# Optimization experiments

Hardware: AMD Instinct MI355X
Metric: run time of the kernel (lower is better)

Reference implementation:

```python
import jax, jax.numpy as jnp
import numpy as np

# Model dims: n_layers, window, n_head, d_head, d_model, d_ff, num_cls, mel_channels, T
L_, W_, H_, DH_ = 8, 32, 8, 64
D_ = H_ * DH_
DFF_, C_, M_, T_ = 2048, 256, 80, 512


def _ln(x, w, b, eps=1e-5):
    mu = x.mean()
    var = ((x - mu) ** 2).mean()
    return (x - mu) * jax.lax.rsqrt(var + eps) * w + b


def setup_inputs() -> dict:
    key = jax.random.key(0)
    ks = jax.random.split(key, 12)
    s = 0.02
    def w(k, shape):
        return jax.random.normal(k, shape, dtype=jnp.float32) * s
    return {
        "y": jax.random.normal(ks[0], (M_, T_), dtype=jnp.float32),
        "samples": jax.random.uniform(ks[1], (T_,), dtype=jnp.float32),
        "emb": jax.random.normal(ks[2], (C_, D_), dtype=jnp.float32),
        "cond_W": w(ks[3], (D_, M_)),
        "ln_w": jnp.ones((L_, D_), jnp.float32),
        "ln_b": jnp.zeros((L_, D_), jnp.float32),
        "kv_w": w(ks[4], (L_, 2 * D_, D_)),
        "kv_b": jnp.zeros((L_, 2 * D_), jnp.float32),
        "q_w": w(ks[5], (L_, D_, D_)),
        "q_b": jnp.zeros((L_, D_), jnp.float32),
        "o_w": w(ks[6], (L_, D_, D_)),
        "o_b": jnp.zeros((L_, D_), jnp.float32),
        "fln_w": jnp.ones((L_, D_), jnp.float32),
        "fln_b": jnp.zeros((L_, D_), jnp.float32),
        "ff_w1": w(ks[7], (L_, DFF_, D_)),
        "ff_b1": jnp.zeros((L_, DFF_), jnp.float32),
        "ff_w2": w(ks[8], (L_, D_, DFF_)),
        "ff_b2": jnp.zeros((L_, D_), jnp.float32),
        "head_r": w(ks[9], (L_, W_, H_, DH_)),
        "last_w": w(ks[10], (C_, D_)),
        "last_b": jnp.zeros((C_,), jnp.float32),
    }


def _decode(y, samples, emb, cond_W, ln_w, ln_b, kv_w, kv_b, q_w, q_b, o_w, o_b,
            fln_w, fln_b, ff_w1, ff_b1, ff_w2, ff_b2, head_r, last_w, last_b):
    L, W, H, Dh = head_r.shape
    D = H * Dh
    C = last_w.shape[0]
    scale = 1.0 / float(np.sqrt(Dh))
    emb_t = jnp.tanh(emb)                 # buffer 'emb' is emb.tanh()
    ycond = (cond_W @ y).T                # [T, D]
    T = ycond.shape[0]
    x0 = emb_t[C // 2 - 1]
    buf0 = jnp.zeros((L, W, 2 * D), ycond.dtype)  # fixed-size rolling KV cache, newest at the end
    layer_params = (ln_w, ln_b, kv_w, kv_b, q_w, q_b, o_w, o_b,
                    fln_w, fln_b, ff_w1, ff_b1, ff_w2, ff_b2, head_r)

    def time_step(carry, ts):
        x, bufs = carry
        cond, sample, t = ts
        # slot w is valid iff it holds a real token: right-aligned, min(t+1, W) valid
        valid = jnp.arange(W) >= (W - 1 - t)

        def layer_step(xc, lp):
            (lw, lb, kw, kb, qw, qb, ow, ob, fw, fb, w1, b1, w2, b2, r, buf) = lp
            xc = cond + xc
            tmp = _ln(xc, lw, lb)
            hkv = kw @ tmp + kb                               # [2D]
            hq = (qw @ tmp + qb).reshape(H, Dh)               # [H, Dh]
            buf = jnp.concatenate([buf[1:], hkv[None]], 0)    # roll cache, [W, 2D]
            k, v = jnp.split(buf, 2, axis=1)
            k = k.reshape(W, H, Dh) + r                       # head_r right-aligned with cache
            v = v.reshape(W, H, Dh)
            scores = jnp.einsum('whd,hd->hw', k, hq) * scale
            scores = jnp.where(valid[None, :], scores, -jnp.inf)
            attn = jax.nn.softmax(scores, axis=1)
            out = jnp.einsum('hw,whd->hd', attn, v).reshape(D)
            xc = ow @ out + ob + xc
            h = jax.nn.gelu(w1 @ _ln(xc, fw, fb) + b1)
            xc = xc + w2 @ h + b2
            return xc, buf

        x, newbufs = jax.lax.scan(layer_step, x, layer_params + (bufs,))
        logits = last_w @ x + last_b                          # c = 1.0
        cum = jnp.cumsum(jax.nn.softmax(logits), axis=0)
        idx = jnp.argmax(cum > sample)                        # first index where cum > u
        return (emb_t[idx], newbufs), (idx, logits)

    (_, _), (outputs, logits) = jax.lax.scan(
        time_step, (x0, buf0), (ycond, samples, jnp.arange(T)))
    return outputs, logits


def reference(y, samples, emb, cond_W, ln_w, ln_b, kv_w, kv_b, q_w, q_b, o_w, o_b,
              fln_w, fln_b, ff_w1, ff_b1, ff_w2, ff_b2, head_r, last_w, last_b):
    outputs, _ = _decode(y, samples, emb, cond_W, ln_w, ln_b, kv_w, kv_b, q_w, q_b,
                         o_w, o_b, fln_w, fln_b, ff_w1, ff_b1, ff_w2, ff_b2,
                         head_r, last_w, last_b)
    return outputs
```

## Files before the change

### kernel.cpp

```cpp
#include <hip/hip_runtime.h>
#include <math.h>

#define LAYERS 8
#define WIN    32
#define NH     8
#define DHD    64
#define DM     512
#define DFF    2048
#define NCLS   256
#define MEL    80
#define TT     512

#define GRID   256
#define BLK    256

#define KVROW  1056

typedef unsigned int  u32;
typedef unsigned long long u64;

__device__ inline float wredsum(float v){
#pragma unroll
  for (int m = 32; m >= 1; m >>= 1) v += __shfl_xor(v, m, 64);
  return v;
}
__device__ inline float wredmax(float v){
#pragma unroll
  for (int m = 32; m >= 1; m >>= 1) v = fmaxf(v, __shfl_xor(v, m, 64));
  return v;
}

__device__ inline float ld_sc(float* p){
  return __hip_atomic_load(p, __ATOMIC_RELAXED, __HIP_MEMORY_SCOPE_AGENT);
}
__device__ inline void st_sc(float* p, float v){
  __hip_atomic_store(p, v, __ATOMIC_RELAXED, __HIP_MEMORY_SCOPE_AGENT);
}
__device__ inline float2 ld_sc2(float* p){
  u64 u = __hip_atomic_load((u64*)p, __ATOMIC_RELAXED, __HIP_MEMORY_SCOPE_AGENT);
  union { u64 u; float2 f; } cv; cv.u = u; return cv.f;
}

__device__ inline float dot512(const float* w, const float* vec, int lane){
  float4 a0 = *(const float4*)(w + 4*lane);
  float4 a1 = *(const float4*)(w + 256 + 4*lane);
  float4 b0 = *(const float4*)(vec + 4*lane);
  float4 b1 = *(const float4*)(vec + 256 + 4*lane);
  float p = a0.x*b0.x + a0.y*b0.y + a0.z*b0.z + a0.w*b0.w
          + a1.x*b1.x + a1.y*b1.y + a1.z*b1.z + a1.w*b1.w;
  return wredsum(p);
}

__device__ inline float gelu_tanh(float x){
  float x3 = x*x*x;
  return 0.5f*x*(1.0f + tanhf(0.7978845608028654f*(x + 0.044715f*x3)));
}

__device__ inline void bar_arrive(u32* flags, int b, int ph){
  __syncthreads();
  if (threadIdx.x == 0)
    __hip_atomic_store(flags + b, (u32)ph, __ATOMIC_RELAXED, __HIP_MEMORY_SCOPE_AGENT);
}
__device__ inline void bar_wait(u32* flags, int ph){
  int tid = threadIdx.x;
  if (tid < 64){
    u64* fp = (u64*)flags + 2*tid;
    for (;;){
      u64 v0 = __hip_atomic_load(fp,     __ATOMIC_RELAXED, __HIP_MEMORY_SCOPE_AGENT);
      u64 v1 = __hip_atomic_load(fp + 1, __ATOMIC_RELAXED, __HIP_MEMORY_SCOPE_AGENT);
      u32 a0 = (u32)v0, a1 = (u32)(v0 >> 32);
      u32 a2 = (u32)v1, a3 = (u32)(v1 >> 32);
      if (min(min(a0, a1), min(a2, a3)) >= (u32)ph) break;
      __builtin_amdgcn_s_sleep(2);
    }
  }
  asm volatile("" ::: "memory");
  __syncthreads();
}

__device__ inline void layernorm512(const float* __restrict__ src,
                                    float* __restrict__ dst,
                                    const float* __restrict__ w,
                                    const float* __restrict__ bb,
                                    int tid, int lane, int wid,
                                    float* s_red, float* s_red2){
  float a = src[tid], c = src[tid + 256];
  float p1 = a + c;
  float p2 = a*a + c*c;
#pragma unroll
  for (int m = 32; m >= 1; m >>= 1){
    p1 += __shfl_xor(p1, m, 64);
    p2 += __shfl_xor(p2, m, 64);
  }
  if (lane == 0){ s_red[wid] = p1; s_red2[wid] = p2; }
  __syncthreads();
  float mu  = (s_red[0]+s_red[1]+s_red[2]+s_red[3])   * (1.0f/512.0f);
  float ex2 = (s_red2[0]+s_red2[1]+s_red2[2]+s_red2[3]) * (1.0f/512.0f);
  float var = fmaxf(ex2 - mu*mu, 0.0f);
  float rsig = 1.0f / sqrtf(var + 1e-5f);
  dst[tid]       = (a - mu)*rsig*w[tid]       + bb[tid];
  dst[tid + 256] = (c - mu)*rsig*w[tid + 256] + bb[tid + 256];
}

__device__ inline void pf_copy(const float* __restrict__ g, float* l, int n4){
  const float4* g4 = (const float4*)g;
  float4* l4 = (float4*)l;
#pragma unroll 4
  for (int i = threadIdx.x; i < n4; i += BLK) l4[i] = g4[i];
}

__device__ inline void pf_kvq(const float* kv_w, const float* q_w, int l, int b, float* s_wA){
  for (int i = threadIdx.x; i < 768; i += BLK){
    int j = i >> 7, off = i & 127;
    int r = b*6 + j;
    float4 v;
    if (r < 2*DM) v = ((const float4*)(kv_w + ((size_t)l*2*DM + r)*DM))[off];
    else          v = ((const float4*)(q_w  + ((size_t)l*DM + (r-2*DM))*DM))[off];
    ((float4*)(s_wA + j*DM))[off] = v;
  }
}

__global__ __launch_bounds__(BLK, 1) void wf_kernel(
    const float* __restrict__ y,      const float* __restrict__ samples,
    const float* __restrict__ emb,    const float* __restrict__ condW,
    const float* __restrict__ ln_w,   const float* __restrict__ ln_b,
    const float* __restrict__ kv_w,   const float* __restrict__ kv_b,
    const float* __restrict__ q_w,    const float* __restrict__ q_b,
    const float* __restrict__ o_w,    const float* __restrict__ o_b,
    const float* __restrict__ fln_w,  const float* __restrict__ fln_b,
    const float* __restrict__ ff_w1,  const float* __restrict__ ff_b1,
    const float* __restrict__ ff_w2,  const float* __restrict__ ff_b2,
    const float* __restrict__ head_r, const float* __restrict__ last_w,
    const float* __restrict__ last_b,
    int* __restrict__ outp, float* __restrict__ ws,
    float* __restrict__ kvhist)
{
  const int tid  = threadIdx.x;
  const int b    = blockIdx.x;
  const int lane = tid & 63;
  const int wid  = tid >> 6;
  const int kz   = b >> 5;
  const int ez0  = (b & 31) * 16;

  u32*   flags  = (u32*)ws;
  float* embt   = ws + 4096;
  float* ycond  = embt + NCLS*DM;
  float* kvc    = ycond + TT*DM;
  float* hq     = kvc + LAYERS*WIN*2*DM;
  float* xpart  = hq + DM;
  float* xc2p   = xpart + 2*8*DM;
  float* logitb = xc2p + 8*DM;
  float* o_wT   = logitb + NCLS;

  __shared__ __align__(16) float s_wA[6*DM];
  __shared__ __align__(16) float s_wB[8*DM];
  __shared__ __align__(16) float s_wC[8*DM];
  __shared__ __align__(16) float s_wO[2*DM];
  __shared__ __align__(16) float s_wL[DM];
  __shared__ __align__(16) float s_xc[DM];
  __shared__ __align__(16) float s_tmp[DM];
  __shared__ __align__(16) float s_q[DHD];
  __shared__ float s_part[BLK];
  __shared__ float s_red[8];
  __shared__ float s_red2[8];
  __shared__ float s_h8[8];
  __shared__ int   s_ired[4];
  __shared__ float s_y[MEL];

  int ph = 0;

  {
    const int gtid = b*BLK + tid;
    for (int i = gtid; i < NCLS*DM; i += GRID*BLK) st_sc(embt + i, tanhf(emb[i]));
  }
  for (int k = 0; k < 2; k++){
    int t0 = b*2 + k;
    if (tid < MEL) s_y[tid] = y[tid*TT + t0];
    __syncthreads();
    for (int dd = tid; dd < DM; dd += BLK){
      const float* cw = condW + dd*MEL;
      float acc = 0.f;
#pragma unroll
      for (int m4 = 0; m4 < MEL; m4 += 4){
        float4 c4 = *(const float4*)(cw + m4);
        acc += c4.x*s_y[m4] + c4.y*s_y[m4+1] + c4.z*s_y[m4+2] + c4.w*s_y[m4+3];
      }
      st_sc(ycond + t0*DM + dd, acc);
    }
    __syncthreads();
  }
  {
    int l = b >> 5, r0 = (b & 31)*16;
    for (int rr = 0; rr < 16; rr++){
      int r = r0 + rr;
      const float* src = o_w + ((size_t)l*DM + r)*DM;
      float v0 = src[tid], v1 = src[tid+256];
      st_sc(o_wT + ((size_t)l*DM + tid)*DM + r, v0);
      st_sc(o_wT + ((size_t)l*DM + tid+256)*DM + r, v1);
    }
  }
  ph++;
  bar_arrive(flags, b, ph);
  pf_kvq(kv_w, q_w, 0, b, s_wA);
  bar_wait(flags, ph);

  int cur_idx = NCLS/2 - 1;
  const float scale = 0.125f;
  const int hh = b >> 5, gg = b & 31;

  for (int t = 0; t < TT; t++){
    float* cond = ycond + t*DM;
    const int slot = t & (WIN-1);
    const int wlo  = (t >= WIN-1) ? 0 : (WIN-1 - t);

    for (int l = 0; l < LAYERS; l++){
      float* xcur = xpart + (l&1)*8*DM;
      float* xnxt = xpart + ((l+1)&1)*8*DM;

      {
        float2 xv;
        if (l == 0){
          xv = *(const float2*)(embt + cur_idx*DM + 2*tid);
        } else {
          xv = make_float2(0.f, 0.f);
#pragma unroll
          for (int k = 0; k < 8; k++){
            float2 p = ld_sc2(xcur + k*DM + 2*tid);
            xv.x += p.x; xv.y += p.y;
          }
        }
        float2 cv = *(const float2*)(cond + 2*tid);
        s_xc[2*tid]   = cv.x + xv.x;
        s_xc[2*tid+1] = cv.y + xv.y;
      }
      __syncthreads();
      layernorm512(s_xc, s_tmp, ln_w + l*DM, ln_b + l*DM, tid, lane, wid, s_red, s_red2);
      __syncthreads();
      {
        if (tid < 16){
          int e = ez0 + tid;
          st_sc(xnxt + kz*DM + e, 0.f);
          float seed = (kz == 0) ? s_xc[e] + o_b[l*DM + e] : 0.f;
          st_sc(xc2p + kz*DM + e, seed);
        }
        float* cacheRow = kvhist ? (kvhist + (size_t)(l*TT + t)*KVROW)
                                 : (kvc + ((size_t)(l*WIN + slot) << 10));
        for (int j = wid; j < 6; j += 4){
          int r = b*6 + j;
          float dv = dot512(s_wA + j*DM, s_tmp, lane);
          if (r < 2*DM){
            dv += kv_b[l*2*DM + r];
            if (lane == 0) st_sc(cacheRow + r, dv);
          } else {
            int rq = r - 2*DM;
            dv += q_b[l*DM + rq];
            if (lane == 0) st_sc(hq + rq, dv);
          }
        }
      }
      ph++;
      bar_arrive(flags, b, ph);
      pf_copy(ff_w1 + ((size_t)l*DFF + b*8)*DM, s_wB, 8*128);
      pf_copy(o_wT + ((size_t)(l*DM + hh*DHD + gg*2))*DM, s_wO, 2*128);
      bar_wait(flags, ph);

      {
        int w = tid >> 3, j = tid & 7;
        float2 k0, k1, k2, k3;
        float2 v2 = make_float2(0.f, 0.f);
        if (kvhist){
          int tp = t - (WIN-1) + w; if (tp < 0) tp = 0;
          const float* kk = kvhist + (size_t)(l*TT + tp)*KVROW + hh*DHD + j*8;
          k0 = *(const float2*)(kk);   k1 = *(const float2*)(kk+2);
          k2 = *(const float2*)(kk+4); k3 = *(const float2*)(kk+6);
          if (tid < 32){
            int tv = t - (WIN-1) + tid; if (tv < 0) tv = 0;
            v2 = *(const float2*)(kvhist + (size_t)(l*TT + tv)*KVROW + DM + hh*DHD + gg*2);
            float2 qv = ld_sc2(hq + hh*DHD + 2*tid);
            s_q[2*tid] = qv.x; s_q[2*tid+1] = qv.y;
          }
        } else {
          int c = (t + 1 + w) & (WIN-1);
          float* kk = kvc + ((size_t)(l*WIN + c) << 10) + hh*DHD + j*8;
          k0 = ld_sc2(kk); k1 = ld_sc2(kk+2); k2 = ld_sc2(kk+4); k3 = ld_sc2(kk+6);
          if (tid < 32){
            int cv2 = (t + 1 + tid) & (WIN-1);
            v2 = ld_sc2(kvc + ((size_t)(l*WIN + cv2) << 10) + DM + hh*DHD + gg*2);
            float2 qv = ld_sc2(hq + hh*DHD + 2*tid);
            s_q[2*tid] = qv.x; s_q[2*tid+1] = qv.y;
          }
        }
        __syncthreads();
        const float* rr = head_r + (((size_t)(l*WIN + w)*NH + hh) << 6) + j*8;
        float2 r0 = *(const float2*)(rr),   r1 = *(const float2*)(rr+2);
        float2 r2 = *(const float2*)(rr+4), r3 = *(const float2*)(rr+6);
        const float* qq = s_q + j*8;
        float acc = (k0.x+r0.x)*qq[0] + (k0.y+r0.y)*qq[1]
                  + (k1.x+r1.x)*qq[2] + (k1.y+r1.y)*qq[3]
                  + (k2.x+r2.x)*qq[4] + (k2.y+r2.y)*qq[5]
                  + (k3.x+r3.x)*qq[6] + (k3.y+r3.y)*qq[7];
        s_part[tid] = acc;
        __syncthreads();
        if (tid < 32){
          float sc = 0.f;
#pragma unroll
          for (int jj = 0; jj < 8; jj++) sc += s_part[tid*8 + jj];
          sc *= scale;
          float sval = (tid >= wlo) ? sc : -INFINITY;
          float m = sval;
#pragma unroll
          for (int mm = 16; mm >= 1; mm >>= 1) m = fmaxf(m, __shfl_xor(m, mm, 64));
          float p = (tid >= wlo) ? expf(sval - m) : 0.f;
          float den = p;
#pragma unroll
          for (int mm = 16; mm >= 1; mm >>= 1) den += __shfl_xor(den, mm, 64);
          float at = p / den;
          float ox = at*v2.x, oy = at*v2.y;
#pragma unroll
          for (int mm = 16; mm >= 1; mm >>= 1){
            ox += __shfl_xor(ox, mm, 64); oy += __shfl_xor(oy, mm, 64);
          }
          if (tid == 0){ s_red[0] = ox; s_red[1] = oy; }
        }
        __syncthreads();
        float o0 = s_red[0], o1 = s_red[1];
        float p0 = s_wO[tid]*o0     + s_wO[DM + tid]*o1;
        float p1 = s_wO[tid+256]*o0 + s_wO[DM + tid+256]*o1;
        unsafeAtomicAdd(xc2p + kz*DM + tid,       p0);
        unsafeAtomicAdd(xc2p + kz*DM + tid + 256, p1);
      }
      ph++;
      bar_arrive(flags, b, ph);
      {
        for (int rr2 = tid; rr2 < DM; rr2 += BLK){
          const float* src = ff_w2 + ((size_t)l*DM + rr2)*DFF + b*8;
          float4 a = *(const float4*)(src);
          float4 c4 = *(const float4*)(src + 4);
          s_wC[0*DM+rr2]=a.x;  s_wC[1*DM+rr2]=a.y;  s_wC[2*DM+rr2]=a.z;  s_wC[3*DM+rr2]=a.w;
          s_wC[4*DM+rr2]=c4.x; s_wC[5*DM+rr2]=c4.y; s_wC[6*DM+rr2]=c4.z; s_wC[7*DM+rr2]=c4.w;
        }
      }
      bar_wait(flags, ph);

      {
        float2 x2 = make_float2(0.f, 0.f);
#pragma unroll
        for (int k = 0; k < 8; k++){
          float2 p = ld_sc2(xc2p + k*DM + 2*tid);
          x2.x += p.x; x2.y += p.y;
        }
        s_xc[2*tid] = x2.x; s_xc[2*tid+1] = x2.y;
      }
      __syncthreads();
      layernorm512(s_xc, s_tmp, fln_w + l*DM, fln_b + l*DM, tid, lane, wid, s_red, s_red2);
      __syncthreads();
      {
        for (int j2 = 0; j2 < 2; j2++){
          int j = wid*2 + j2;
          float dv = dot512(s_wB + j*DM, s_tmp, lane) + ff_b1[l*DFF + b*8 + j];
          if (lane == 0) s_h8[j] = gelu_tanh(dv);
        }
      }
      __syncthreads();
      {
        float h0=s_h8[0], h1=s_h8[1], h2=s_h8[2], h3=s_h8[3];
        float h4=s_h8[4], h5=s_h8[5], h6=s_h8[6], h7=s_h8[7];
        int r0 = tid, r1 = tid + 256;
        float p0 = s_wC[r0]*h0 + s_wC[DM+r0]*h1 + s_wC[2*DM+r0]*h2 + s_wC[3*DM+r0]*h3
                 + s_wC[4*DM+r0]*h4 + s_wC[5*DM+r0]*h5 + s_wC[6*DM+r0]*h6 + s_wC[7*DM+r0]*h7;
        float p1 = s_wC[r1]*h0 + s_wC[DM+r1]*h1 + s_wC[2*DM+r1]*h2 + s_wC[3*DM+r1]*h3
                 + s_wC[4*DM+r1]*h4 + s_wC[5*DM+r1]*h5 + s_wC[6*DM+r1]*h6 + s_wC[7*DM+r1]*h7;
        if (r0 == b*2)     p0 += s_xc[r0] + ff_b2[l*DM + r0];
        if (r0 == b*2 + 1) p0 += s_xc[r0] + ff_b2[l*DM + r0];
        if (r1 == b*2)     p1 += s_xc[r1] + ff_b2[l*DM + r1];
        if (r1 == b*2 + 1) p1 += s_xc[r1] + ff_b2[l*DM + r1];
        unsafeAtomicAdd(xnxt + kz*DM + r0, p0);
        unsafeAtomicAdd(xnxt + kz*DM + r1, p1);
      }
      ph++;
      bar_arrive(flags, b, ph);
      if (l < LAYERS-1) pf_kvq(kv_w, q_w, l+1, b, s_wA);
      else              pf_copy(last_w + (size_t)b*DM, s_wL, 128);
      bar_wait(flags, ph);
    }

    {
      float2 xv = make_float2(0.f, 0.f);
#pragma unroll
      for (int k = 0; k < 8; k++){
        float2 p = ld_sc2(xpart + k*DM + 2*tid);
        xv.x += p.x; xv.y += p.y;
      }
      s_tmp[2*tid] = xv.x; s_tmp[2*tid+1] = xv.y;
    }
    __syncthreads();
    if (wid == 0){
      float dv = dot512(s_wL, s_tmp, lane) + last_b[b];
      if (lane == 0) st_sc(logitb + b, dv);
    }
    ph++;
    bar_arrive(flags, b, ph);
    pf_kvq(kv_w, q_w, 0, b, s_wA);
    bar_wait(flags, ph);

    {
      float u  = samples[t];
      float li = ld_sc(logitb + tid);
      float mx = wredmax(li);
      if (lane == 0) s_red[wid] = mx;
      __syncthreads();
      mx = fmaxf(fmaxf(s_red[0], s_red[1]), fmaxf(s_red[2], s_red[3]));
      float p  = expf(li - mx);
      float sm = wredsum(p);
      __syncthreads();
      if (lane == 0) s_red[wid] = sm;
      __syncthreads();
      float den = s_red[0]+s_red[1]+s_red[2]+s_red[3];
      float q = p / den;
      float x = q;
#pragma unroll
      for (int off = 1; off < 64; off <<= 1){
        float n = __shfl_up(x, off, 64);
        if (lane >= off) x += n;
      }
      __syncthreads();
      if (lane == 63) s_red[wid] = x;
      __syncthreads();
      float offs = 0.f;
      for (int j2 = 0; j2 < wid; j2++) offs += s_red[j2];
      float cum = x + offs;
      unsigned long long bal = __ballot(cum > u);
      int first = (bal != 0ULL) ? (__ffsll(bal) - 1) : 9999;
      if (lane == 0) s_ired[wid] = (first < 9999) ? (wid*64 + first) : 9999;
      __syncthreads();
      int idx = min(min(s_ired[0], s_ired[1]), min(s_ired[2], s_ired[3]));
      if (idx == 9999) idx = 0;
      cur_idx = idx;
      if (b == 0 && tid == 0) outp[t] = idx;
      __syncthreads();
    }
  }
}

extern "C" void kernel_launch(void* const* d_in, const int* in_sizes, int n_in,
                              void* d_out, int out_size, void* d_ws, size_t ws_size,
                              hipStream_t stream)
{
  (void)in_sizes; (void)n_in; (void)out_size;
  hipMemsetAsync(d_ws, 0, 2048, stream);

  const float* y      = (const float*)d_in[0];
  const float* samp   = (const float*)d_in[1];
  const float* emb    = (const float*)d_in[2];
  const float* condW  = (const float*)d_in[3];
  const float* ln_w   = (const float*)d_in[4];
  const float* ln_b   = (const float*)d_in[5];
  const float* kv_w   = (const float*)d_in[6];
  const float* kv_b   = (const float*)d_in[7];
  const float* q_w    = (const float*)d_in[8];
  const float* q_b    = (const float*)d_in[9];
  const float* o_w    = (const float*)d_in[10];
  const float* o_b    = (const float*)d_in[11];
  const float* fln_w  = (const float*)d_in[12];
  const float* fln_b  = (const float*)d_in[13];
  const float* ff_w1  = (const float*)d_in[14];
  const float* ff_b1  = (const float*)d_in[15];
  const float* ff_w2  = (const float*)d_in[16];
  const float* ff_b2  = (const float*)d_in[17];
  const float* head_r = (const float*)d_in[18];
  const float* last_w = (const float*)d_in[19];
  const float* last_b = (const float*)d_in[20];

  const size_t baseFloats = 4096 + (size_t)NCLS*DM + (size_t)TT*DM
                          + (size_t)LAYERS*WIN*2*DM + DM + 2*8*DM + 8*DM + NCLS
                          + (size_t)LAYERS*DM*DM;
  const size_t histFloats = (size_t)LAYERS*TT*KVROW;
  const size_t needBytes  = (baseFloats + histFloats) * sizeof(float);
  float* kvhist = (ws_size >= needBytes) ? ((float*)d_ws + baseFloats) : nullptr;

  wf_kernel<<<GRID, BLK, 0, stream>>>(y, samp, emb, condW, ln_w, ln_b, kv_w, kv_b,
                                      q_w, q_b, o_w, o_b, fln_w, fln_b,
                                      ff_w1, ff_b1, ff_w2, ff_b2, head_r,
                                      last_w, last_b,
                                      (int*)d_out, (float*)d_ws, kvhist);
}
```

Baseline: 57.23 ms.

## Pre-transpose ff_w2 slices once and prefetch weights with warps 1-3 only

Adds a one-time prologue that writes each block's ff_w2 column slice, already transposed, into a contiguous workspace region, so the per-layer prefetch becomes a plain float4 copy instead of a strided gather. All weight prefetch helpers now skip wave 0 and split the copy over the other 192 threads, likely to keep wave 0 free for barrier polling and to overlap the barrier wait. This costs extra workspace and a larger prologue, and is used only when the workspace is big enough.

```diff
diff --git a/kernel.cpp b/kernel.cpp
--- a/kernel.cpp
+++ b/kernel.cpp
@@ -102,15 +102,16 @@
   dst[tid + 256] = (c - mu)*rsig*w[tid + 256] + bb[tid + 256];
 }
 
-__device__ inline void pf_copy(const float* __restrict__ g, float* l, int n4){
+__device__ inline void pf_copy192(const float* __restrict__ g, float* l, int n4){
+  if (threadIdx.x < 64) return;
   const float4* g4 = (const float4*)g;
   float4* l4 = (float4*)l;
-#pragma unroll 4
-  for (int i = threadIdx.x; i < n4; i += BLK) l4[i] = g4[i];
-}
-
-__device__ inline void pf_kvq(const float* kv_w, const float* q_w, int l, int b, float* s_wA){
-  for (int i = threadIdx.x; i < 768; i += BLK){
+  for (int i = (int)threadIdx.x - 64; i < n4; i += 192) l4[i] = g4[i];
+}
+
+__device__ inline void pf_kvq192(const float* kv_w, const float* q_w, int l, int b, float* s_wA){
+  if (threadIdx.x < 64) return;
+  for (int i = (int)threadIdx.x - 64; i < 768; i += 192){
     int j = i >> 7, off = i & 127;
     int r = b*6 + j;
     float4 v;
@@ -133,7 +134,8 @@
     const float* __restrict__ head_r, const float* __restrict__ last_w,
     const float* __restrict__ last_b,
     int* __restrict__ outp, float* __restrict__ ws,
-    float* __restrict__ kvhist)
+    float* __restrict__ kvhist,
+    float* __restrict__ w2T)
 {
   const int tid  = threadIdx.x;
   const int b    = blockIdx.x;
@@ -199,9 +201,21 @@
       st_sc(o_wT + ((size_t)l*DM + tid+256)*DM + r, v1);
     }
   }
+  if (w2T){
+    for (int l2 = 0; l2 < LAYERS; l2++){
+      float* dst = w2T + ((size_t)(l2*GRID + b))*8*DM;
+      for (int r = tid; r < DM; r += BLK){
+        const float* src = ff_w2 + ((size_t)l2*DM + r)*DFF + b*8;
+        float4 a = *(const float4*)(src);
+        float4 c4 = *(const float4*)(src + 4);
+        dst[0*DM+r]=a.x;  dst[1*DM+r]=a.y;  dst[2*DM+r]=a.z;  dst[3*DM+r]=a.w;
+        dst[4*DM+r]=c4.x; dst[5*DM+r]=c4.y; dst[6*DM+r]=c4.z; dst[7*DM+r]=c4.w;
+      }
+    }
+  }
   ph++;
   bar_arrive(flags, b, ph);
-  pf_kvq(kv_w, q_w, 0, b, s_wA);
+  pf_kvq192(kv_w, q_w, 0, b, s_wA);
   bar_wait(flags, ph);
 
   int cur_idx = NCLS/2 - 1;
@@ -260,8 +274,8 @@
       }
       ph++;
       bar_arrive(flags, b, ph);
-      pf_copy(ff_w1 + ((size_t)l*DFF + b*8)*DM, s_wB, 8*128);
-      pf_copy(o_wT + ((size_t)(l*DM + hh*DHD + gg*2))*DM, s_wO, 2*128);
+      pf_copy192(ff_w1 + ((size_t)l*DFF + b*8)*DM, s_wB, 8*128);
+      pf_copy192(o_wT + ((size_t)(l*DM + hh*DHD + gg*2))*DM, s_wO, 2*128);
       bar_wait(flags, ph);
 
       {
@@ -331,13 +345,17 @@
       }
       ph++;
       bar_arrive(flags, b, ph);
-      {
-        for (int rr2 = tid; rr2 < DM; rr2 += BLK){
-          const float* src = ff_w2 + ((size_t)l*DM + rr2)*DFF + b*8;
-          float4 a = *(const float4*)(src);
-          float4 c4 = *(const float4*)(src + 4);
-          s_wC[0*DM+rr2]=a.x;  s_wC[1*DM+rr2]=a.y;  s_wC[2*DM+rr2]=a.z;  s_wC[3*DM+rr2]=a.w;
-          s_wC[4*DM+rr2]=c4.x; s_wC[5*DM+rr2]=c4.y; s_wC[6*DM+rr2]=c4.z; s_wC[7*DM+rr2]=c4.w;
+      if (w2T){
+        pf_copy192(w2T + ((size_t)(l*GRID + b))*8*DM, s_wC, 8*128);
+      } else {
+        if (tid >= 64){
+          for (int rr2 = tid - 64; rr2 < DM; rr2 += 192){
+            const float* src = ff_w2 + ((size_t)l*DM + rr2)*DFF + b*8;
+            float4 a = *(const float4*)(src);
+            float4 c4 = *(const float4*)(src + 4);
+            s_wC[0*DM+rr2]=a.x;  s_wC[1*DM+rr2]=a.y;  s_wC[2*DM+rr2]=a.z;  s_wC[3*DM+rr2]=a.w;
+            s_wC[4*DM+rr2]=c4.x; s_wC[5*DM+rr2]=c4.y; s_wC[6*DM+rr2]=c4.z; s_wC[7*DM+rr2]=c4.w;
+          }
         }
       }
       bar_wait(flags, ph);
@@ -379,8 +397,8 @@
       }
       ph++;
       bar_arrive(flags, b, ph);
-      if (l < LAYERS-1) pf_kvq(kv_w, q_w, l+1, b, s_wA);
-      else              pf_copy(last_w + (size_t)b*DM, s_wL, 128);
+      if (l < LAYERS-1) pf_kvq192(kv_w, q_w, l+1, b, s_wA);
+      else              pf_copy192(last_w + (size_t)b*DM, s_wL, 128);
       bar_wait(flags, ph);
     }
 
@@ -400,7 +418,7 @@
     }
     ph++;
     bar_arrive(flags, b, ph);
-    pf_kvq(kv_w, q_w, 0, b, s_wA);
+    pf_kvq192(kv_w, q_w, 0, b, s_wA);
     bar_wait(flags, ph);
 
     {
@@ -475,12 +493,15 @@
                           + (size_t)LAYERS*WIN*2*DM + DM + 2*8*DM + 8*DM + NCLS
                           + (size_t)LAYERS*DM*DM;
   const size_t histFloats = (size_t)LAYERS*TT*KVROW;
-  const size_t needBytes  = (baseFloats + histFloats) * sizeof(float);
-  float* kvhist = (ws_size >= needBytes) ? ((float*)d_ws + baseFloats) : nullptr;
+  const size_t w2tFloats  = (size_t)LAYERS*GRID*8*DM;
+  const size_t needHist   = (baseFloats + histFloats) * sizeof(float);
+  const size_t needW2T    = (baseFloats + histFloats + w2tFloats) * sizeof(float);
+  float* kvhist = (ws_size >= needHist) ? ((float*)d_ws + baseFloats) : nullptr;
+  float* w2T    = (ws_size >= needW2T)  ? ((float*)d_ws + baseFloats + histFloats) : nullptr;
 
   wf_kernel<<<GRID, BLK, 0, stream>>>(y, samp, emb, condW, ln_w, ln_b, kv_w, kv_b,
                                       q_w, q_b, o_w, o_b, fln_w, fln_b,
                                       ff_w1, ff_b1, ff_w2, ff_b2, head_r,
                                       last_w, last_b,
-                                      (int*)d_out, (float*)d_ws, kvhist);
-}
+                                      (int*)d_out, (float*)d_ws, kvhist, w2T);
+}
```

After: 85.57 ms. +49.5%, slower.
